# Kernel optimization log

Measured on AMD Instinct MI355X. Metric: run time of the kernel, lower is better.

Reference implementation:

```python
import jax, jax.numpy as jnp
import numpy as np

B, C, T = 32, 1024, 1024
BETA = 0.95      # snn.Leaky(beta=0.95)
THR = 1.0        # snntorch Leaky default threshold
SIGMA_INIT = 10.5  # mean of sigma_range (1, 20)


def _gaussian_matrix(sigma, channels):
    # row i is the Gaussian pdf over x=0..C-1 centered at mean=i (vectorized
    # form of the source's per-row Python loop; identical values).
    x = jnp.arange(channels, dtype=jnp.float32)
    u = (x[None, :] - x[:, None]) / sigma  # [C, C]
    coef = 1.0 / (sigma * jnp.sqrt(jnp.asarray(2.0 * jnp.pi, dtype=jnp.float32)))
    return coef * jnp.exp(-0.5 * u * u)


def _spike(u):
    # heaviside(u) forward; ATan surrogate gradient (snntorch default, alpha=2)
    soft = jnp.arctan(jnp.pi * u) / jnp.pi
    hard = (u > 0).astype(u.dtype)
    return soft + jax.lax.stop_gradient(hard - soft)


def setup_inputs() -> dict:
    key = jax.random.key(0)
    inp = jax.random.normal(key, (B, C, T), dtype=jnp.float32)
    sigma = jnp.ones((1,), dtype=jnp.float32) * SIGMA_INIT
    return {"inp": inp, "sigma": sigma}


def reference(inp, sigma):
    # inp: [B, C, T], sigma: [1]
    s = sigma[0]
    w = _gaussian_matrix(s, inp.shape[1])  # computed once: identical at every t
    # I[b,i,t] = x[b,i,t] - sum_j w[i,j] * x[b,j,t]
    I = inp - jnp.einsum('ij,bjt->bit', w, inp)
    I_tbc = jnp.moveaxis(I, 2, 0)  # [T, B, C]

    def step(mem, It):
        # snntorch Leaky (reset_mechanism='subtract'):
        # reset fires on incoming mem, then decay+integrate, then spike.
        reset = _spike(mem - THR)
        mem = BETA * mem + It - reset * THR
        spk = _spike(mem - THR)
        return mem, spk

    mem0 = jnp.zeros(I_tbc.shape[1:], dtype=inp.dtype)  # [B, C]
    _, spks = jax.lax.scan(step, mem0, I_tbc)  # spks: [T, B, C]
    return jnp.moveaxis(spks, 0, 2)  # [B, C, T]
```

## Files before the change

kernel.cpp:

```cpp
#include <hip/hip_runtime.h>
#include <math.h>

#define B_     32
#define C_     1024
#define T_     1024
#define RT     92
#define CT     64
#define TT     64
#define KC     8
#define NTY    8
#define WOFF   (RT + KC - 1)
#define NWT    200
#define NCOLS  (CT + 2*RT)
#define XSTR   252
#define ISTR   68
#define NF4    (NCOLS * (TT/4))
#define NSQ0   19
#define NSQN   12

__device__ __forceinline__ float tap_value(float s, int d) {
    float u    = __fdiv_rn((float)d, s);
    float t1   = __fmul_rn(-0.5f, u);
    float t2   = __fmul_rn(t1, u);
    float e    = (float)exp((double)t2);
    float den  = __fmul_rn(s, sqrtf(6.2831854820251465f));
    float coef = __fdiv_rn(1.0f, den);
    return __fmul_rn(coef, e);
}

#define EL(v, i) ((i) == 0 ? (v).x : (i) == 1 ? (v).y : (i) == 2 ? (v).z : (v).w)
#define SEL5(il, T0, T1, T2, T3, T4)                                            \
    ((il) < 4 ? EL(T0, (il)) : (il) < 8 ? EL(T1, (il) - 4)                      \
     : (il) < 12 ? EL(T2, (il) - 8) : (il) < 16 ? EL(T3, (il) - 12)             \
     : EL(T4, (il) - 16))

#define COL(XV, CC, T0, T1, T2, T3, T4)                                         \
    do {                                                                        \
        float x1_ = EL(XV, (CC) & 3);                                           \
        _Pragma("unroll")                                                       \
        for (int k = 0; k < KC; ++k) {                                          \
            const int il_ = (CC) + 7 - k;                                       \
            acc[k] = fmaf(SEL5(il_, T0, T1, T2, T3, T4), x1_, acc[k]);          \
        }                                                                       \
    } while (0)

#define GETQ(Q)                                                                 \
    (((Q) >= NSQ0 && (Q) < NSQ0 + NSQN)                                         \
         ? sgq[((Q) >= NSQ0 && (Q) < NSQ0 + NSQN) ? (Q) - NSQ0 : 0]             \
         : TAPQ(Q))

#define PASSX(QB, T0, T1, T2, T3, T4, L0, L1, L2, XA, XB, XC, YA, YB, YC, DOLD) \
    do {                                                                        \
        if (DOLD) {                                                             \
            YA = xq[(QB) + 3]; YB = xq[(QB) + 4]; YC = xq[(QB) + 5];            \
            L0 = GETQ((QB) + 5); L1 = GETQ((QB) + 6); L2 = GETQ((QB) + 7);      \
        }                                                                       \
        COL(XA, 0, T0, T1, T2, T3, T4);  COL(XA, 1, T0, T1, T2, T3, T4);        \
        COL(XA, 2, T0, T1, T2, T3, T4);  COL(XA, 3, T0, T1, T2, T3, T4);        \
        COL(XB, 4, T0, T1, T2, T3, T4);  COL(XB, 5, T0, T1, T2, T3, T4);        \
        COL(XB, 6, T0, T1, T2, T3, T4);  COL(XB, 7, T0, T1, T2, T3, T4);        \
        COL(XC, 8, T0, T1, T2, T3, T4);  COL(XC, 9, T0, T1, T2, T3, T4);        \
        COL(XC, 10, T0, T1, T2, T3, T4); COL(XC, 11, T0, T1, T2, T3, T4);       \
    } while (0)

__global__ __launch_bounds__(512, 4) void snn_v16(
    const float* __restrict__ x, const float* __restrict__ sigma,
    float* __restrict__ out)
{
    __shared__ __align__(16) float xsT[TT * XSTR];
    __shared__ __align__(16) float IsS[NTY * KC * ISTR];

    const int tx   = threadIdx.x;
    const int ty   = threadIdx.y;
    const int flat = ty * 64 + tx;
    const int b    = blockIdx.y;
    const int c0   = blockIdx.x * CT;
    const int rb   = ty * KC;

    const float* xb = x   + (size_t)b * ((size_t)C_ * T_);
    float*       ob = out + (size_t)b * ((size_t)C_ * T_);

    if (flat < NWT) {
        int d = flat - WOFF;
        xsT[(flat >> 2) * XSTR + 248 + (flat & 3)] =
            (d >= -RT && d <= RT) ? tap_value(sigma[0], d) : 0.0f;
    }

    float4 stg[2][4];
    const int rB  = (flat >> 2);
    const int c4B = (flat & 3);

#define STAGE_LOAD(T0)                                                          \
    _Pragma("unroll")                                                           \
    for (int i1 = 0; i1 < 2; ++i1) {                                            \
        _Pragma("unroll")                                                       \
        for (int i2 = 0; i2 < 4; ++i2) {                                        \
            int r  = rB + 128 * i1;                                             \
            int c4 = c4B + 4 * i2;                                              \
            int c  = c0 - RT + r;                                               \
            float4 v = make_float4(0.f, 0.f, 0.f, 0.f);                         \
            if (r < NCOLS && c >= 0 && c < C_)                                  \
                v = *(const float4*)(xb + (size_t)c * T_ + (T0) + c4 * 4);      \
            stg[i1][i2] = v;                                                    \
        }                                                                       \
    }

#define STAGE_WRITE()                                                           \
    _Pragma("unroll")                                                           \
    for (int i1 = 0; i1 < 2; ++i1) {                                            \
        _Pragma("unroll")                                                       \
        for (int i2 = 0; i2 < 4; ++i2) {                                        \
            int r  = rB + 128 * i1;                                             \
            int c4 = c4B + 4 * i2;                                              \
            if (r < NCOLS) {                                                    \
                xsT[(4 * c4 + 0) * XSTR + r] = stg[i1][i2].x;                   \
                xsT[(4 * c4 + 1) * XSTR + r] = stg[i1][i2].y;                   \
                xsT[(4 * c4 + 2) * XSTR + r] = stg[i1][i2].z;                   \
                xsT[(4 * c4 + 3) * XSTR + r] = stg[i1][i2].w;                   \
            }                                                                   \
        }                                                                       \
    }

#define TAPQ(Q) (*(const float4*)(xsT + (Q) * XSTR + 248))

    STAGE_LOAD(0);
    __syncthreads();

    float4 sgq[NSQN];
#pragma unroll
    for (int i = 0; i < NSQN; ++i) {
        float4 q = TAPQ(NSQ0 + i);
        sgq[i].x = __int_as_float(__builtin_amdgcn_readfirstlane(__float_as_int(q.x)));
        sgq[i].y = __int_as_float(__builtin_amdgcn_readfirstlane(__float_as_int(q.y)));
        sgq[i].z = __int_as_float(__builtin_amdgcn_readfirstlane(__float_as_int(q.z)));
        sgq[i].w = __int_as_float(__builtin_amdgcn_readfirstlane(__float_as_int(q.w)));
    }

    float mem = 0.0f;
    float rc  = 0.0f;
    float* strip = IsS + ty * (KC * ISTR);
    const float4* xq = (const float4*)(xsT + tx * XSTR + rb);

#pragma unroll 1
    for (int kk = 0; kk < T_ / TT; ++kk) {
        STAGE_WRITE();
        __syncthreads();

        if (kk < T_ / TT - 1) { STAGE_LOAD((kk + 1) * TT); }

        float acc[KC];
#pragma unroll
        for (int k = 0; k < KC; ++k) acc[k] = 0.0f;

        float4 n0 = GETQ(0), n1 = GETQ(1), n2 = GETQ(2), n3 = GETQ(3), n4 = GETQ(4);
        float4 x0 = xq[0], x1 = xq[1], x2 = xq[2];
        float4 n5, n6, n7, x3, x4, x5;

        PASSX(0,  n0,n1,n2,n3,n4, n5,n6,n7, x0,x1,x2, x3,x4,x5, 1);
        PASSX(3,  n3,n4,n5,n6,n7, n0,n1,n2, x3,x4,x5, x0,x1,x2, 1);
        PASSX(6,  n6,n7,n0,n1,n2, n3,n4,n5, x0,x1,x2, x3,x4,x5, 1);
        PASSX(9,  n1,n2,n3,n4,n5, n6,n7,n0, x3,x4,x5, x0,x1,x2, 1);
        PASSX(12, n4,n5,n6,n7,n0, n1,n2,n3, x0,x1,x2, x3,x4,x5, 1);
        PASSX(15, n7,n0,n1,n2,n3, n4,n5,n6, x3,x4,x5, x0,x1,x2, 1);
        PASSX(18, n2,n3,n4,n5,n6, n7,n0,n1, x0,x1,x2, x3,x4,x5, 1);
        PASSX(21, n5,n6,n7,n0,n1, n2,n3,n4, x3,x4,x5, x0,x1,x2, 1);
        PASSX(24, n0,n1,n2,n3,n4, n5,n6,n7, x0,x1,x2, x3,x4,x5, 1);
        PASSX(27, n3,n4,n5,n6,n7, n0,n1,n2, x3,x4,x5, x0,x1,x2, 1);
        PASSX(30, n6,n7,n0,n1,n2, n3,n4,n5, x0,x1,x2, x3,x4,x5, 1);
        PASSX(33, n1,n2,n3,n4,n5, n6,n7,n0, x3,x4,x5, x0,x1,x2, 1);
        PASSX(36, n4,n5,n6,n7,n0, n1,n2,n3, x0,x1,x2, x3,x4,x5, 1);
        PASSX(39, n7,n0,n1,n2,n3, n4,n5,n6, x3,x4,x5, x0,x1,x2, 1);
        PASSX(42, n2,n3,n4,n5,n6, n7,n0,n1, x0,x1,x2, x3,x4,x5, 1);
        PASSX(45, n5,n6,n7,n0,n1, n2,n3,n4, x3,x4,x5, x0,x1,x2, 0);

        {
            float4 xo0 = xq[RT / 4];
            float4 xo1 = xq[RT / 4 + 1];
            strip[0 * ISTR + tx] = __fsub_rn(xo0.x, acc[0]);
            strip[1 * ISTR + tx] = __fsub_rn(xo0.y, acc[1]);
            strip[2 * ISTR + tx] = __fsub_rn(xo0.z, acc[2]);
            strip[3 * ISTR + tx] = __fsub_rn(xo0.w, acc[3]);
            strip[4 * ISTR + tx] = __fsub_rn(xo1.x, acc[4]);
            strip[5 * ISTR + tx] = __fsub_rn(xo1.y, acc[5]);
            strip[6 * ISTR + tx] = __fsub_rn(xo1.z, acc[6]);
            strip[7 * ISTR + tx] = __fsub_rn(xo1.w, acc[7]);
        }

        if (tx < KC) {
            float m = mem, r = rc;
            const float4* srow4 = (const float4*)(strip + tx * ISTR);
            float* orow = ob + (size_t)(c0 + rb + tx) * T_ + (size_t)kk * TT;
#pragma unroll 4
            for (int q = 0; q < TT / 4; ++q) {
                float4 Iq = srow4[q];
                float4 s;
#pragma unroll
                for (int qq = 0; qq < 4; ++qq) {
                    float Ivv = EL(Iq, qq);
                    m = __fsub_rn(__fadd_rn(__fmul_rn(0.95f, m), Ivv), r);
                    float sp = (m > 1.0f) ? 1.0f : 0.0f;
                    r = sp;
                    if (qq == 0) s.x = sp; else if (qq == 1) s.y = sp;
                    else if (qq == 2) s.z = sp; else s.w = sp;
                }
                *(float4*)(orow + 4 * q) = s;
            }
            mem = m; rc = r;
        }
        __syncthreads();
    }
#undef STAGE_LOAD
#undef STAGE_WRITE
#undef TAPQ
}

extern "C" void kernel_launch(void* const* d_in, const int* in_sizes, int n_in,
                              void* d_out, int out_size, void* d_ws, size_t ws_size,
                              hipStream_t stream) {
    const float* x     = (const float*)d_in[0];
    const float* sigma = (const float*)d_in[1];
    float* out = (float*)d_out;

    dim3 grid(C_ / CT, B_);
    dim3 block(64, NTY);

    snn_v16<<<grid, block, 0, stream>>>(x, sigma, out);
}
```

Before: 177.4 us.

## Split fused conv+LIF kernel into parallel conv pass and separate scan pass

Replaces the single kernel that looped over time tiles with a convolution kernel gridded over channel, time and batch tiles that writes I into the output buffer. A second kernel then reads I back and runs the sequential leaky integrate-and-fire scan in place. Gaussian taps can be precomputed once into workspace by a tiny init kernel. This aims to expose far more parallelism for the convolution, at the cost of an extra full round trip of I through global memory and two additional launches.

```diff
diff --git a/kernel.cpp b/kernel.cpp
--- a/kernel.cpp
+++ b/kernel.cpp
@@ -5,18 +5,15 @@
 #define C_     1024
 #define T_     1024
 #define RT     92
-#define CT     64
-#define TT     64
 #define KC     8
-#define NTY    8
 #define WOFF   (RT + KC - 1)
 #define NWT    200
-#define NCOLS  (CT + 2*RT)
-#define XSTR   252
-#define ISTR   68
-#define NF4    (NCOLS * (TT/4))
-#define NSQ0   19
-#define NSQN   12
+
+#define P1_CT   256
+#define P1_TT   16
+#define P1_NC   (P1_CT + 2*RT)
+#define P1_XSTR 444
+#define P1_NF4  (P1_NC * (P1_TT/4))
 
 __device__ __forceinline__ float tap_value(float s, int d) {
     float u    = __fdiv_rn((float)d, s);
@@ -26,6 +23,14 @@
     float den  = __fmul_rn(s, sqrtf(6.2831854820251465f));
     float coef = __fdiv_rn(1.0f, den);
     return __fmul_rn(coef, e);
+}
+
+__global__ void init_w_kernel(const float* __restrict__ sigma, float* __restrict__ gw) {
+    int i = threadIdx.x;
+    if (i < NWT) {
+        int d = i - WOFF;
+        gw[i] = (d >= -RT && d <= RT) ? tap_value(sigma[0], d) : 0.0f;
+    }
 }
 
 #define EL(v, i) ((i) == 0 ? (v).x : (i) == 1 ? (v).y : (i) == 2 ? (v).z : (v).w)
@@ -44,10 +49,8 @@
         }                                                                       \
     } while (0)
 
-#define GETQ(Q)                                                                 \
-    (((Q) >= NSQ0 && (Q) < NSQ0 + NSQN)                                         \
-         ? sgq[((Q) >= NSQ0 && (Q) < NSQ0 + NSQN) ? (Q) - NSQ0 : 0]             \
-         : TAPQ(Q))
+#define GETQ(Q) (((Q) >= 19 && (Q) < 31) ? sgq[((Q) >= 19 && (Q) < 31) ? (Q) - 19 : 0] \
+                                         : wt4[(Q)])
 
 #define PASSX(QB, T0, T1, T2, T3, T4, L0, L1, L2, XA, XB, XC, YA, YB, YC, DOLD) \
     do {                                                                        \
@@ -63,140 +66,140 @@
         COL(XC, 10, T0, T1, T2, T3, T4); COL(XC, 11, T0, T1, T2, T3, T4);       \
     } while (0)
 
-__global__ __launch_bounds__(512, 4) void snn_v16(
+template <bool GW>
+__global__ __launch_bounds__(512, 8) void snn_conv_I(
     const float* __restrict__ x, const float* __restrict__ sigma,
-    float* __restrict__ out)
+    const float* __restrict__ gw, float* __restrict__ out)
 {
-    __shared__ __align__(16) float xsT[TT * XSTR];
-    __shared__ __align__(16) float IsS[NTY * KC * ISTR];
+    __shared__ __align__(16) float xsT[P1_TT * P1_XSTR];
+    __shared__ __align__(16) float wtab[NWT];
 
     const int tx   = threadIdx.x;
     const int ty   = threadIdx.y;
-    const int flat = ty * 64 + tx;
-    const int b    = blockIdx.y;
-    const int c0   = blockIdx.x * CT;
+    const int flat = ty * 16 + tx;
+    const int c0   = blockIdx.x * P1_CT;
+    const int t0   = blockIdx.y * P1_TT;
+    const int b    = blockIdx.z;
     const int rb   = ty * KC;
 
-    const float* xb = x   + (size_t)b * ((size_t)C_ * T_);
-    float*       ob = out + (size_t)b * ((size_t)C_ * T_);
+    const float* xb = x + (size_t)b * ((size_t)C_ * T_);
 
     if (flat < NWT) {
-        int d = flat - WOFF;
-        xsT[(flat >> 2) * XSTR + 248 + (flat & 3)] =
-            (d >= -RT && d <= RT) ? tap_value(sigma[0], d) : 0.0f;
-    }
-
-    float4 stg[2][4];
-    const int rB  = (flat >> 2);
-    const int c4B = (flat & 3);
-
-#define STAGE_LOAD(T0)                                                          \
-    _Pragma("unroll")                                                           \
-    for (int i1 = 0; i1 < 2; ++i1) {                                            \
-        _Pragma("unroll")                                                       \
-        for (int i2 = 0; i2 < 4; ++i2) {                                        \
-            int r  = rB + 128 * i1;                                             \
-            int c4 = c4B + 4 * i2;                                              \
-            int c  = c0 - RT + r;                                               \
-            float4 v = make_float4(0.f, 0.f, 0.f, 0.f);                         \
-            if (r < NCOLS && c >= 0 && c < C_)                                  \
-                v = *(const float4*)(xb + (size_t)c * T_ + (T0) + c4 * 4);      \
-            stg[i1][i2] = v;                                                    \
-        }                                                                       \
-    }
-
-#define STAGE_WRITE()                                                           \
-    _Pragma("unroll")                                                           \
-    for (int i1 = 0; i1 < 2; ++i1) {                                            \
-        _Pragma("unroll")                                                       \
-        for (int i2 = 0; i2 < 4; ++i2) {                                        \
-            int r  = rB + 128 * i1;                                             \
-            int c4 = c4B + 4 * i2;                                              \
-            if (r < NCOLS) {                                                    \
-                xsT[(4 * c4 + 0) * XSTR + r] = stg[i1][i2].x;                   \
-                xsT[(4 * c4 + 1) * XSTR + r] = stg[i1][i2].y;                   \
-                xsT[(4 * c4 + 2) * XSTR + r] = stg[i1][i2].z;                   \
-                xsT[(4 * c4 + 3) * XSTR + r] = stg[i1][i2].w;                   \
-            }                                                                   \
-        }                                                                       \
-    }
-
-#define TAPQ(Q) (*(const float4*)(xsT + (Q) * XSTR + 248))
-
-    STAGE_LOAD(0);
+        if (GW) wtab[flat] = gw[flat];
+        else {
+            int d = flat - WOFF;
+            wtab[flat] = (d >= -RT && d <= RT) ? tap_value(sigma[0], d) : 0.0f;
+        }
+    }
+
+#pragma unroll
+    for (int i = 0; i < 4; ++i) {
+        int e = flat + i * 512;
+        if (e < P1_NF4) {
+            int r = e >> 2, c4 = e & 3;
+            int c = c0 - RT + r;
+            float4 v = make_float4(0.f, 0.f, 0.f, 0.f);
+            if (c >= 0 && c < C_)
+                v = *(const float4*)(xb + (size_t)c * T_ + t0 + c4 * 4);
+            xsT[(4 * c4 + 0) * P1_XSTR + r] = v.x;
+            xsT[(4 * c4 + 1) * P1_XSTR + r] = v.y;
+            xsT[(4 * c4 + 2) * P1_XSTR + r] = v.z;
+            xsT[(4 * c4 + 3) * P1_XSTR + r] = v.w;
+        }
+    }
     __syncthreads();
 
-    float4 sgq[NSQN];
-#pragma unroll
-    for (int i = 0; i < NSQN; ++i) {
-        float4 q = TAPQ(NSQ0 + i);
+    const float4* wt4 = (const float4*)wtab;
+    float4 sgq[12];
+#pragma unroll
+    for (int i = 0; i < 12; ++i) {
+        float4 q = wt4[19 + i];
         sgq[i].x = __int_as_float(__builtin_amdgcn_readfirstlane(__float_as_int(q.x)));
         sgq[i].y = __int_as_float(__builtin_amdgcn_readfirstlane(__float_as_int(q.y)));
         sgq[i].z = __int_as_float(__builtin_amdgcn_readfirstlane(__float_as_int(q.z)));
         sgq[i].w = __int_as_float(__builtin_amdgcn_readfirstlane(__float_as_int(q.w)));
     }
 
+    float acc[KC];
+#pragma unroll
+    for (int k = 0; k < KC; ++k) acc[k] = 0.0f;
+
+    const float4* xq = (const float4*)(xsT + tx * P1_XSTR + rb);
+
+    float4 n0 = GETQ(0), n1 = GETQ(1), n2 = GETQ(2), n3 = GETQ(3), n4 = GETQ(4);
+    float4 x0 = xq[0], x1 = xq[1], x2 = xq[2];
+    float4 n5, n6, n7, x3, x4, x5;
+
+    PASSX(0,  n0,n1,n2,n3,n4, n5,n6,n7, x0,x1,x2, x3,x4,x5, 1);
+    PASSX(3,  n3,n4,n5,n6,n7, n0,n1,n2, x3,x4,x5, x0,x1,x2, 1);
+    PASSX(6,  n6,n7,n0,n1,n2, n3,n4,n5, x0,x1,x2, x3,x4,x5, 1);
+    PASSX(9,  n1,n2,n3,n4,n5, n6,n7,n0, x3,x4,x5, x0,x1,x2, 1);
+    PASSX(12, n4,n5,n6,n7,n0, n1,n2,n3, x0,x1,x2, x3,x4,x5, 1);
+    PASSX(15, n7,n0,n1,n2,n3, n4,n5,n6, x3,x4,x5, x0,x1,x2, 1);
+    PASSX(18, n2,n3,n4,n5,n6, n7,n0,n1, x0,x1,x2, x3,x4,x5, 1);
+    PASSX(21, n5,n6,n7,n0,n1, n2,n3,n4, x3,x4,x5, x0,x1,x2, 1);
+    PASSX(24, n0,n1,n2,n3,n4, n5,n6,n7, x0,x1,x2, x3,x4,x5, 1);
+    PASSX(27, n3,n4,n5,n6,n7, n0,n1,n2, x3,x4,x5, x0,x1,x2, 1);
+    PASSX(30, n6,n7,n0,n1,n2, n3,n4,n5, x0,x1,x2, x3,x4,x5, 1);
+    PASSX(33, n1,n2,n3,n4,n5, n6,n7,n0, x3,x4,x5, x0,x1,x2, 1);
+    PASSX(36, n4,n5,n6,n7,n0, n1,n2,n3, x0,x1,x2, x3,x4,x5, 1);
+    PASSX(39, n7,n0,n1,n2,n3, n4,n5,n6, x3,x4,x5, x0,x1,x2, 1);
+    PASSX(42, n2,n3,n4,n5,n6, n7,n0,n1, x0,x1,x2, x3,x4,x5, 1);
+    PASSX(45, n5,n6,n7,n0,n1, n2,n3,n4, x3,x4,x5, x0,x1,x2, 0);
+
+    {
+        float4 xo0 = xq[RT / 4];
+        float4 xo1 = xq[RT / 4 + 1];
+        float Iv[KC] = {
+            __fsub_rn(xo0.x, acc[0]), __fsub_rn(xo0.y, acc[1]),
+            __fsub_rn(xo0.z, acc[2]), __fsub_rn(xo0.w, acc[3]),
+            __fsub_rn(xo1.x, acc[4]), __fsub_rn(xo1.y, acc[5]),
+            __fsub_rn(xo1.z, acc[6]), __fsub_rn(xo1.w, acc[7])};
+        float* obase = out + ((size_t)b * C_ + (c0 + rb)) * T_ + t0 + tx;
+#pragma unroll
+        for (int k = 0; k < KC; ++k)
+            obase[(size_t)k * T_] = Iv[k];
+    }
+}
+
+__global__ __launch_bounds__(512) void snn_scan(float* __restrict__ out)
+{
+    __shared__ float Is[64 * 65];
+
+    const int tx   = threadIdx.x;
+    const int ty   = threadIdx.y;
+    const int flat = ty * 64 + tx;
+    const int c0   = blockIdx.x * 64;
+    const int b    = blockIdx.y;
+
+    float* base = out + ((size_t)b * C_ + c0) * T_;
+
     float mem = 0.0f;
     float rc  = 0.0f;
-    float* strip = IsS + ty * (KC * ISTR);
-    const float4* xq = (const float4*)(xsT + tx * XSTR + rb);
 
 #pragma unroll 1
-    for (int kk = 0; kk < T_ / TT; ++kk) {
-        STAGE_WRITE();
+    for (int kk = 0; kk < T_ / 64; ++kk) {
+#pragma unroll
+        for (int i = 0; i < 2; ++i) {
+            int e = flat + i * 512;
+            int r = e >> 4, c4 = e & 15;
+            float4 v = *(const float4*)(base + (size_t)r * T_ + kk * 64 + c4 * 4);
+            Is[r * 65 + 4 * c4 + 0] = v.x;
+            Is[r * 65 + 4 * c4 + 1] = v.y;
+            Is[r * 65 + 4 * c4 + 2] = v.z;
+            Is[r * 65 + 4 * c4 + 3] = v.w;
+        }
         __syncthreads();
 
-        if (kk < T_ / TT - 1) { STAGE_LOAD((kk + 1) * TT); }
-
-        float acc[KC];
-#pragma unroll
-        for (int k = 0; k < KC; ++k) acc[k] = 0.0f;
-
-        float4 n0 = GETQ(0), n1 = GETQ(1), n2 = GETQ(2), n3 = GETQ(3), n4 = GETQ(4);
-        float4 x0 = xq[0], x1 = xq[1], x2 = xq[2];
-        float4 n5, n6, n7, x3, x4, x5;
-
-        PASSX(0,  n0,n1,n2,n3,n4, n5,n6,n7, x0,x1,x2, x3,x4,x5, 1);
-        PASSX(3,  n3,n4,n5,n6,n7, n0,n1,n2, x3,x4,x5, x0,x1,x2, 1);
-        PASSX(6,  n6,n7,n0,n1,n2, n3,n4,n5, x0,x1,x2, x3,x4,x5, 1);
-        PASSX(9,  n1,n2,n3,n4,n5, n6,n7,n0, x3,x4,x5, x0,x1,x2, 1);
-        PASSX(12, n4,n5,n6,n7,n0, n1,n2,n3, x0,x1,x2, x3,x4,x5, 1);
-        PASSX(15, n7,n0,n1,n2,n3, n4,n5,n6, x3,x4,x5, x0,x1,x2, 1);
-        PASSX(18, n2,n3,n4,n5,n6, n7,n0,n1, x0,x1,x2, x3,x4,x5, 1);
-        PASSX(21, n5,n6,n7,n0,n1, n2,n3,n4, x3,x4,x5, x0,x1,x2, 1);
-        PASSX(24, n0,n1,n2,n3,n4, n5,n6,n7, x0,x1,x2, x3,x4,x5, 1);
-        PASSX(27, n3,n4,n5,n6,n7, n0,n1,n2, x3,x4,x5, x0,x1,x2, 1);
-        PASSX(30, n6,n7,n0,n1,n2, n3,n4,n5, x0,x1,x2, x3,x4,x5, 1);
-        PASSX(33, n1,n2,n3,n4,n5, n6,n7,n0, x3,x4,x5, x0,x1,x2, 1);
-        PASSX(36, n4,n5,n6,n7,n0, n1,n2,n3, x0,x1,x2, x3,x4,x5, 1);
-        PASSX(39, n7,n0,n1,n2,n3, n4,n5,n6, x3,x4,x5, x0,x1,x2, 1);
-        PASSX(42, n2,n3,n4,n5,n6, n7,n0,n1, x0,x1,x2, x3,x4,x5, 1);
-        PASSX(45, n5,n6,n7,n0,n1, n2,n3,n4, x3,x4,x5, x0,x1,x2, 0);
-
-        {
-            float4 xo0 = xq[RT / 4];
-            float4 xo1 = xq[RT / 4 + 1];
-            strip[0 * ISTR + tx] = __fsub_rn(xo0.x, acc[0]);
-            strip[1 * ISTR + tx] = __fsub_rn(xo0.y, acc[1]);
-            strip[2 * ISTR + tx] = __fsub_rn(xo0.z, acc[2]);
-            strip[3 * ISTR + tx] = __fsub_rn(xo0.w, acc[3]);
-            strip[4 * ISTR + tx] = __fsub_rn(xo1.x, acc[4]);
-            strip[5 * ISTR + tx] = __fsub_rn(xo1.y, acc[5]);
-            strip[6 * ISTR + tx] = __fsub_rn(xo1.z, acc[6]);
-            strip[7 * ISTR + tx] = __fsub_rn(xo1.w, acc[7]);
-        }
-
-        if (tx < KC) {
+        if (ty == 0) {
             float m = mem, r = rc;
-            const float4* srow4 = (const float4*)(strip + tx * ISTR);
-            float* orow = ob + (size_t)(c0 + rb + tx) * T_ + (size_t)kk * TT;
+            float* orow = base + (size_t)tx * T_ + kk * 64;
 #pragma unroll 4
-            for (int q = 0; q < TT / 4; ++q) {
-                float4 Iq = srow4[q];
+            for (int q = 0; q < 16; ++q) {
                 float4 s;
 #pragma unroll
                 for (int qq = 0; qq < 4; ++qq) {
-                    float Ivv = EL(Iq, qq);
+                    float Ivv = Is[tx * 65 + 4 * q + qq];
                     m = __fsub_rn(__fadd_rn(__fmul_rn(0.95f, m), Ivv), r);
                     float sp = (m > 1.0f) ? 1.0f : 0.0f;
                     r = sp;
@@ -209,9 +212,6 @@
         }
         __syncthreads();
     }
-#undef STAGE_LOAD
-#undef STAGE_WRITE
-#undef TAPQ
 }
 
 extern "C" void kernel_launch(void* const* d_in, const int* in_sizes, int n_in,
@@ -221,8 +221,17 @@
     const float* sigma = (const float*)d_in[1];
     float* out = (float*)d_out;
 
-    dim3 grid(C_ / CT, B_);
-    dim3 block(64, NTY);
-
-    snn_v16<<<grid, block, 0, stream>>>(x, sigma, out);
-}
+    dim3 g1(C_ / P1_CT, T_ / P1_TT, B_);
+    dim3 b1(P1_TT, 32);
+    dim3 g2(C_ / 64, B_);
+    dim3 b2(64, 8);
+
+    if (ws_size >= NWT * sizeof(float)) {
+        float* gw = (float*)d_ws;
+        init_w_kernel<<<1, 256, 0, stream>>>(sigma, gw);
+        snn_conv_I<true><<<g1, b1, 0, stream>>>(x, sigma, gw, out);
+    } else {
+        snn_conv_I<false><<<g1, b1, 0, stream>>>(x, sigma, nullptr, out);
+    }
+    snn_scan<<<g2, b2, 0, stream>>>(out);
+}
```

Measured after the change: 214.5 us. 20.9% more time.

## Split block into ping-pong warp groups overlapping convolution, scan, and loads

Applied to the files above, without the earlier changes.

Splits the block into two four-wave groups that alternate by time chunk. One group computes the Gaussian convolution for a 32-step chunk while the other runs the serial LIF scan and reloads its double buffer for the next chunk. The membrane state now lives in LDS, and the scan uses 64 lanes instead of 8. The aim is to hide the serial scan and global loads behind convolution math, at the cost of half the convolution threads being idle per phase and twice as many barriers.

```diff
diff --git a/kernel.cpp b/kernel.cpp
--- a/kernel.cpp
+++ b/kernel.cpp
@@ -5,16 +5,14 @@
 #define C_     1024
 #define T_     1024
 #define RT     92
-#define CT     64
-#define TT     64
 #define KC     8
-#define NTY    8
 #define WOFF   (RT + KC - 1)
 #define NWT    200
-#define NCOLS  (CT + 2*RT)
+#define NCOLS  248
 #define XSTR   252
-#define ISTR   68
-#define NF4    (NCOLS * (TT/4))
+#define TTC    32
+#define ISTR   33
+#define NQ4    (NCOLS * (TTC/4))
 #define NSQ0   19
 #define NSQN   12
 
@@ -44,6 +42,8 @@
         }                                                                       \
     } while (0)
 
+#define TAPQ(Q)                                                                 \
+    (*(const float4*)(((Q) < 32 ? xsA + (Q) * XSTR : xsB + ((Q) - 32) * XSTR) + 248))
 #define GETQ(Q)                                                                 \
     (((Q) >= NSQ0 && (Q) < NSQ0 + NSQN)                                         \
          ? sgq[((Q) >= NSQ0 && (Q) < NSQ0 + NSQN) ? (Q) - NSQ0 : 0]             \
@@ -63,67 +63,51 @@
         COL(XC, 10, T0, T1, T2, T3, T4); COL(XC, 11, T0, T1, T2, T3, T4);       \
     } while (0)
 
-__global__ __launch_bounds__(512, 4) void snn_v16(
+__global__ __launch_bounds__(512, 4) void snn_v19(
     const float* __restrict__ x, const float* __restrict__ sigma,
     float* __restrict__ out)
 {
-    __shared__ __align__(16) float xsT[TT * XSTR];
-    __shared__ __align__(16) float IsS[NTY * KC * ISTR];
+    __shared__ __align__(16) float xsA[TTC * XSTR];
+    __shared__ __align__(16) float xsB[TTC * XSTR];
+    __shared__ __align__(16) float stripA[64 * ISTR];
+    __shared__ __align__(16) float stripB[64 * ISTR];
+    __shared__ float mem_lds[64];
 
     const int tx   = threadIdx.x;
     const int ty   = threadIdx.y;
     const int flat = ty * 64 + tx;
+    const int g    = ty >> 2;
+    const int wg   = ty & 3;
     const int b    = blockIdx.y;
-    const int c0   = blockIdx.x * CT;
-    const int rb   = ty * KC;
+    const int c0   = blockIdx.x * 64;
 
     const float* xb = x   + (size_t)b * ((size_t)C_ * T_);
     float*       ob = out + (size_t)b * ((size_t)C_ * T_);
 
     if (flat < NWT) {
         int d = flat - WOFF;
-        xsT[(flat >> 2) * XSTR + 248 + (flat & 3)] =
-            (d >= -RT && d <= RT) ? tap_value(sigma[0], d) : 0.0f;
-    }
-
-    float4 stg[2][4];
-    const int rB  = (flat >> 2);
-    const int c4B = (flat & 3);
-
-#define STAGE_LOAD(T0)                                                          \
-    _Pragma("unroll")                                                           \
-    for (int i1 = 0; i1 < 2; ++i1) {                                            \
-        _Pragma("unroll")                                                       \
-        for (int i2 = 0; i2 < 4; ++i2) {                                        \
-            int r  = rB + 128 * i1;                                             \
-            int c4 = c4B + 4 * i2;                                              \
-            int c  = c0 - RT + r;                                               \
-            float4 v = make_float4(0.f, 0.f, 0.f, 0.f);                         \
-            if (r < NCOLS && c >= 0 && c < C_)                                  \
-                v = *(const float4*)(xb + (size_t)c * T_ + (T0) + c4 * 4);      \
-            stg[i1][i2] = v;                                                    \
-        }                                                                       \
-    }
-
-#define STAGE_WRITE()                                                           \
-    _Pragma("unroll")                                                           \
-    for (int i1 = 0; i1 < 2; ++i1) {                                            \
-        _Pragma("unroll")                                                       \
-        for (int i2 = 0; i2 < 4; ++i2) {                                        \
-            int r  = rB + 128 * i1;                                             \
-            int c4 = c4B + 4 * i2;                                              \
-            if (r < NCOLS) {                                                    \
-                xsT[(4 * c4 + 0) * XSTR + r] = stg[i1][i2].x;                   \
-                xsT[(4 * c4 + 1) * XSTR + r] = stg[i1][i2].y;                   \
-                xsT[(4 * c4 + 2) * XSTR + r] = stg[i1][i2].z;                   \
-                xsT[(4 * c4 + 3) * XSTR + r] = stg[i1][i2].w;                   \
-            }                                                                   \
-        }                                                                       \
-    }
-
-#define TAPQ(Q) (*(const float4*)(xsT + (Q) * XSTR + 248))
-
-    STAGE_LOAD(0);
+        float w = (d >= -RT && d <= RT) ? tap_value(sigma[0], d) : 0.0f;
+        int q = flat >> 2, e = flat & 3;
+        float* dst = (q < 32) ? (xsA + q * XSTR + 248 + e)
+                              : (xsB + (q - 32) * XSTR + 248 + e);
+        *dst = w;
+    }
+    if (flat < 64) mem_lds[flat] = 0.0f;
+#pragma unroll
+    for (int i = 0; i < 4; ++i) {
+        int e = flat + i * 512;
+        if (e < NQ4) {
+            int r = e >> 3, c4 = e & 7;
+            int c = c0 - RT + r;
+            float4 v = make_float4(0.f, 0.f, 0.f, 0.f);
+            if (c >= 0 && c < C_)
+                v = *(const float4*)(xb + (size_t)c * T_ + c4 * 4);
+            xsA[(4 * c4 + 0) * XSTR + r] = v.x;
+            xsA[(4 * c4 + 1) * XSTR + r] = v.y;
+            xsA[(4 * c4 + 2) * XSTR + r] = v.z;
+            xsA[(4 * c4 + 3) * XSTR + r] = v.w;
+        }
+    }
     __syncthreads();
 
     float4 sgq[NSQN];
@@ -136,82 +120,106 @@
         sgq[i].w = __int_as_float(__builtin_amdgcn_readfirstlane(__float_as_int(q.w)));
     }
 
-    float mem = 0.0f;
-    float rc  = 0.0f;
-    float* strip = IsS + ty * (KC * ISTR);
-    const float4* xq = (const float4*)(xsT + tx * XSTR + rb);
+    const int tloc = tx & 31;
+    const int rb   = wg * 16 + (tx >> 5) * 8;
+    float* bufg    = (g == 0) ? xsA : xsB;
+    float* stripg  = (g == 0) ? stripA : stripB;
+    const float4* xq = (const float4*)(bufg + tloc * XSTR + rb);
 
 #pragma unroll 1
-    for (int kk = 0; kk < T_ / TT; ++kk) {
-        STAGE_WRITE();
-        __syncthreads();
-
-        if (kk < T_ / TT - 1) { STAGE_LOAD((kk + 1) * TT); }
-
-        float acc[KC];
-#pragma unroll
-        for (int k = 0; k < KC; ++k) acc[k] = 0.0f;
-
-        float4 n0 = GETQ(0), n1 = GETQ(1), n2 = GETQ(2), n3 = GETQ(3), n4 = GETQ(4);
-        float4 x0 = xq[0], x1 = xq[1], x2 = xq[2];
-        float4 n5, n6, n7, x3, x4, x5;
-
-        PASSX(0,  n0,n1,n2,n3,n4, n5,n6,n7, x0,x1,x2, x3,x4,x5, 1);
-        PASSX(3,  n3,n4,n5,n6,n7, n0,n1,n2, x3,x4,x5, x0,x1,x2, 1);
-        PASSX(6,  n6,n7,n0,n1,n2, n3,n4,n5, x0,x1,x2, x3,x4,x5, 1);
-        PASSX(9,  n1,n2,n3,n4,n5, n6,n7,n0, x3,x4,x5, x0,x1,x2, 1);
-        PASSX(12, n4,n5,n6,n7,n0, n1,n2,n3, x0,x1,x2, x3,x4,x5, 1);
-        PASSX(15, n7,n0,n1,n2,n3, n4,n5,n6, x3,x4,x5, x0,x1,x2, 1);
-        PASSX(18, n2,n3,n4,n5,n6, n7,n0,n1, x0,x1,x2, x3,x4,x5, 1);
-        PASSX(21, n5,n6,n7,n0,n1, n2,n3,n4, x3,x4,x5, x0,x1,x2, 1);
-        PASSX(24, n0,n1,n2,n3,n4, n5,n6,n7, x0,x1,x2, x3,x4,x5, 1);
-        PASSX(27, n3,n4,n5,n6,n7, n0,n1,n2, x3,x4,x5, x0,x1,x2, 1);
-        PASSX(30, n6,n7,n0,n1,n2, n3,n4,n5, x0,x1,x2, x3,x4,x5, 1);
-        PASSX(33, n1,n2,n3,n4,n5, n6,n7,n0, x3,x4,x5, x0,x1,x2, 1);
-        PASSX(36, n4,n5,n6,n7,n0, n1,n2,n3, x0,x1,x2, x3,x4,x5, 1);
-        PASSX(39, n7,n0,n1,n2,n3, n4,n5,n6, x3,x4,x5, x0,x1,x2, 1);
-        PASSX(42, n2,n3,n4,n5,n6, n7,n0,n1, x0,x1,x2, x3,x4,x5, 1);
-        PASSX(45, n5,n6,n7,n0,n1, n2,n3,n4, x3,x4,x5, x0,x1,x2, 0);
-
-        {
+    for (int m = 0; m <= 32; ++m) {
+        if (m <= 31 && g == (m & 1)) {
+            float acc[KC];
+#pragma unroll
+            for (int k = 0; k < KC; ++k) acc[k] = 0.0f;
+
+            float4 n0 = GETQ(0), n1 = GETQ(1), n2 = GETQ(2), n3 = GETQ(3), n4 = GETQ(4);
+            float4 x0 = xq[0], x1 = xq[1], x2 = xq[2];
+            float4 n5, n6, n7, x3, x4, x5;
+
+            PASSX(0,  n0,n1,n2,n3,n4, n5,n6,n7, x0,x1,x2, x3,x4,x5, 1);
+            PASSX(3,  n3,n4,n5,n6,n7, n0,n1,n2, x3,x4,x5, x0,x1,x2, 1);
+            PASSX(6,  n6,n7,n0,n1,n2, n3,n4,n5, x0,x1,x2, x3,x4,x5, 1);
+            PASSX(9,  n1,n2,n3,n4,n5, n6,n7,n0, x3,x4,x5, x0,x1,x2, 1);
+            PASSX(12, n4,n5,n6,n7,n0, n1,n2,n3, x0,x1,x2, x3,x4,x5, 1);
+            PASSX(15, n7,n0,n1,n2,n3, n4,n5,n6, x3,x4,x5, x0,x1,x2, 1);
+            PASSX(18, n2,n3,n4,n5,n6, n7,n0,n1, x0,x1,x2, x3,x4,x5, 1);
+            PASSX(21, n5,n6,n7,n0,n1, n2,n3,n4, x3,x4,x5, x0,x1,x2, 1);
+            PASSX(24, n0,n1,n2,n3,n4, n5,n6,n7, x0,x1,x2, x3,x4,x5, 1);
+            PASSX(27, n3,n4,n5,n6,n7, n0,n1,n2, x3,x4,x5, x0,x1,x2, 1);
+            PASSX(30, n6,n7,n0,n1,n2, n3,n4,n5, x0,x1,x2, x3,x4,x5, 1);
+            PASSX(33, n1,n2,n3,n4,n5, n6,n7,n0, x3,x4,x5, x0,x1,x2, 1);
+            PASSX(36, n4,n5,n6,n7,n0, n1,n2,n3, x0,x1,x2, x3,x4,x5, 1);
+            PASSX(39, n7,n0,n1,n2,n3, n4,n5,n6, x3,x4,x5, x0,x1,x2, 1);
+            PASSX(42, n2,n3,n4,n5,n6, n7,n0,n1, x0,x1,x2, x3,x4,x5, 1);
+            PASSX(45, n5,n6,n7,n0,n1, n2,n3,n4, x3,x4,x5, x0,x1,x2, 0);
+
             float4 xo0 = xq[RT / 4];
             float4 xo1 = xq[RT / 4 + 1];
-            strip[0 * ISTR + tx] = __fsub_rn(xo0.x, acc[0]);
-            strip[1 * ISTR + tx] = __fsub_rn(xo0.y, acc[1]);
-            strip[2 * ISTR + tx] = __fsub_rn(xo0.z, acc[2]);
-            strip[3 * ISTR + tx] = __fsub_rn(xo0.w, acc[3]);
-            strip[4 * ISTR + tx] = __fsub_rn(xo1.x, acc[4]);
-            strip[5 * ISTR + tx] = __fsub_rn(xo1.y, acc[5]);
-            strip[6 * ISTR + tx] = __fsub_rn(xo1.z, acc[6]);
-            strip[7 * ISTR + tx] = __fsub_rn(xo1.w, acc[7]);
-        }
-
-        if (tx < KC) {
-            float m = mem, r = rc;
-            const float4* srow4 = (const float4*)(strip + tx * ISTR);
-            float* orow = ob + (size_t)(c0 + rb + tx) * T_ + (size_t)kk * TT;
-#pragma unroll 4
-            for (int q = 0; q < TT / 4; ++q) {
-                float4 Iq = srow4[q];
-                float4 s;
-#pragma unroll
-                for (int qq = 0; qq < 4; ++qq) {
-                    float Ivv = EL(Iq, qq);
-                    m = __fsub_rn(__fadd_rn(__fmul_rn(0.95f, m), Ivv), r);
-                    float sp = (m > 1.0f) ? 1.0f : 0.0f;
-                    r = sp;
-                    if (qq == 0) s.x = sp; else if (qq == 1) s.y = sp;
-                    else if (qq == 2) s.z = sp; else s.w = sp;
+            stripg[(rb + 0) * ISTR + tloc] = __fsub_rn(xo0.x, acc[0]);
+            stripg[(rb + 1) * ISTR + tloc] = __fsub_rn(xo0.y, acc[1]);
+            stripg[(rb + 2) * ISTR + tloc] = __fsub_rn(xo0.z, acc[2]);
+            stripg[(rb + 3) * ISTR + tloc] = __fsub_rn(xo0.w, acc[3]);
+            stripg[(rb + 4) * ISTR + tloc] = __fsub_rn(xo1.x, acc[4]);
+            stripg[(rb + 5) * ISTR + tloc] = __fsub_rn(xo1.y, acc[5]);
+            stripg[(rb + 6) * ISTR + tloc] = __fsub_rn(xo1.z, acc[6]);
+            stripg[(rb + 7) * ISTR + tloc] = __fsub_rn(xo1.w, acc[7]);
+        } else {
+            if (wg == 0) {
+                if (m >= 1 && g == ((m - 1) & 1)) {
+                    float mv = mem_lds[tx];
+                    float r  = (mv > 1.0f) ? 1.0f : 0.0f;
+                    const float* srow = stripg + tx * ISTR;
+                    float* orow = ob + (size_t)(c0 + tx) * T_ + (size_t)(m - 1) * TTC;
+#pragma unroll
+                    for (int q = 0; q < TTC / 4; ++q) {
+                        float4 s;
+#pragma unroll
+                        for (int qq = 0; qq < 4; ++qq) {
+                            float Ivv = srow[4 * q + qq];
+                            mv = __fsub_rn(__fadd_rn(__fmul_rn(0.95f, mv), Ivv), r);
+                            float sp = (mv > 1.0f) ? 1.0f : 0.0f;
+                            r = sp;
+                            if (qq == 0) s.x = sp; else if (qq == 1) s.y = sp;
+                            else if (qq == 2) s.z = sp; else s.w = sp;
+                        }
+                        *(float4*)(orow + 4 * q) = s;
+                    }
+                    mem_lds[tx] = mv;
                 }
-                *(float4*)(orow + 4 * q) = s;
+            } else {
+                if (m + 1 <= 31) {
+                    const int t0s  = (m + 1) * TTC;
+                    const int wthr = (wg - 1) * 64 + tx;
+                    float4 vv[11];
+#pragma unroll
+                    for (int i = 0; i < 11; ++i) {
+                        int e = wthr + i * 192;
+                        float4 v = make_float4(0.f, 0.f, 0.f, 0.f);
+                        if (e < NQ4) {
+                            int r = e >> 3, c4 = e & 7;
+                            int c = c0 - RT + r;
+                            if (c >= 0 && c < C_)
+                                v = *(const float4*)(xb + (size_t)c * T_ + t0s + c4 * 4);
+                        }
+                        vv[i] = v;
+                    }
+#pragma unroll
+                    for (int i = 0; i < 11; ++i) {
+                        int e = wthr + i * 192;
+                        if (e < NQ4) {
+                            int r = e >> 3, c4 = e & 7;
+                            bufg[(4 * c4 + 0) * XSTR + r] = vv[i].x;
+                            bufg[(4 * c4 + 1) * XSTR + r] = vv[i].y;
+                            bufg[(4 * c4 + 2) * XSTR + r] = vv[i].z;
+                            bufg[(4 * c4 + 3) * XSTR + r] = vv[i].w;
+                        }
+                    }
+                }
             }
-            mem = m; rc = r;
         }
         __syncthreads();
     }
-#undef STAGE_LOAD
-#undef STAGE_WRITE
-#undef TAPQ
 }
 
 extern "C" void kernel_launch(void* const* d_in, const int* in_sizes, int n_in,
@@ -221,8 +229,8 @@
     const float* sigma = (const float*)d_in[1];
     float* out = (float*)d_out;
 
-    dim3 grid(C_ / CT, B_);
-    dim3 block(64, NTY);
-
-    snn_v16<<<grid, block, 0, stream>>>(x, sigma, out);
+    dim3 grid(C_ / 64, B_);
+    dim3 block(64, 8);
+
+    snn_v19<<<grid, block, 0, stream>>>(x, sigma, out);
 }
```

Result: faster. 166.3 us (-6.3%).
